# Kernel tuning notes

Hardware: AMD Instinct MI355X
Metric: run time of the kernel (lower is better)

## Reference

```python
import jax, jax.numpy as jnp
import numpy as np

B, T = 32, 1024
VOCAB, N_POS = 300, 3001
D, N_HEAD, D_HID, L = 256, 2, 1024, 4
K1_PAD = 4  # kernel 9, padding 4; second conv is kernel 1, padding 0
EPS = 1e-5


def layer_norm(x, g, b):
    m = jnp.mean(x, axis=-1, keepdims=True)
    v = jnp.mean((x - m) ** 2, axis=-1, keepdims=True)
    return (x - m) * jax.lax.rsqrt(v + EPS) * g + b


def setup_inputs() -> dict:
    key = jax.random.key(0)
    ks = jax.random.split(key, 16)
    src_seq = jax.random.randint(ks[0], (B, T), 0, VOCAB)
    src_pos = jnp.broadcast_to(jnp.arange(1, T + 1), (B, T)).astype(jnp.int32)
    word_emb = (0.02 * jax.random.normal(ks[1], (VOCAB, D))).at[0].set(0.0)  # padding_idx=0
    pos_emb = (0.02 * jax.random.normal(ks[2], (N_POS, D))).at[0].set(0.0)
    s = 0.02
    qkv_w = np.sqrt(2.0 / (D + D // N_HEAD)) * jax.random.normal(ks[3], (L, 3 * D, D))
    qkv_b = jnp.zeros((L, 3 * D))
    fc_w = s * jax.random.normal(ks[4], (L, D, D))
    fc_b = jnp.zeros((L, D))
    ln1_g = jnp.ones((L, D)); ln1_b = jnp.zeros((L, D))
    conv1_w = s * jax.random.normal(ks[5], (L, D_HID, D, 9))
    conv1_b = jnp.zeros((L, D_HID))
    conv2_w = s * jax.random.normal(ks[6], (L, D, D_HID, 1))
    conv2_b = jnp.zeros((L, D))
    ln2_g = jnp.ones((L, D)); ln2_b = jnp.zeros((L, D))
    return dict(src_seq=src_seq, src_pos=src_pos, word_emb=word_emb, pos_emb=pos_emb,
                qkv_w=qkv_w, qkv_b=qkv_b, fc_w=fc_w, fc_b=fc_b,
                ln1_g=ln1_g, ln1_b=ln1_b, conv1_w=conv1_w, conv1_b=conv1_b,
                conv2_w=conv2_w, conv2_b=conv2_b, ln2_g=ln2_g, ln2_b=ln2_b)


def encoder(src_seq, src_pos, word_emb, pos_emb, qkv_w, qkv_b, fc_w, fc_b,
            ln1_g, ln1_b, conv1_w, conv1_b, conv2_w, conv2_b, ln2_g, ln2_b):
    non_pad = (src_seq != 0).astype(jnp.float32)[..., None]          # [B,T,1]
    key_pad = (src_seq == 0)[:, None, None, :]                        # [B,1,1,T]
    x = word_emb[src_seq] + pos_emb[src_pos]                          # [B,T,D]
    dk = D // N_HEAD

    def block(x, p):
        qw, qb, fw, fb, g1, be1, w1, b1, w2, b2, g2, be2 = p
        res = x
        h = layer_norm(x, g1, be1)
        qkv = h @ qw.T + qb                                           # [B,T,3D]
        q, k, v = jnp.split(qkv, 3, axis=-1)
        split = lambda t: t.reshape(B, T, N_HEAD, dk).transpose(0, 2, 1, 3)
        q, k, v = split(q), split(k), split(v)
        attn = jnp.einsum('bhqd,bhkd->bhqk', q, k) / jnp.sqrt(jnp.float32(dk))
        attn = jnp.where(key_pad, -jnp.inf, attn)
        attn = jax.nn.softmax(attn, axis=-1)
        o = jnp.einsum('bhqk,bhkd->bhqd', attn, v)
        o = o.transpose(0, 2, 1, 3).reshape(B, T, D)
        x = (o @ fw.T + fb) + res
        x = x * non_pad
        # position-wise conv FFN
        res = x
        h = layer_norm(x, g2, be2).transpose(0, 2, 1)                 # [B,D,T]
        h = jax.lax.conv_general_dilated(h, w1, (1,), [(K1_PAD, K1_PAD)],
                                         dimension_numbers=('NCH', 'OIH', 'NCH'))
        h = jax.nn.relu(h + b1[None, :, None])
        h = jax.lax.conv_general_dilated(h, w2, (1,), [(0, 0)],
                                         dimension_numbers=('NCH', 'OIH', 'NCH'))
        h = h + b2[None, :, None]
        x = h.transpose(0, 2, 1) + res
        x = x * non_pad
        return x, None

    params = (qkv_w, qkv_b, fc_w, fc_b, ln1_g, ln1_b,
              conv1_w, conv1_b, conv2_w, conv2_b, ln2_g, ln2_b)
    x, _ = jax.lax.scan(block, x, params)
    return x, non_pad


def reference(src_seq, src_pos, word_emb, pos_emb, qkv_w, qkv_b, fc_w, fc_b,
              ln1_g, ln1_b, conv1_w, conv1_b, conv2_w, conv2_b, ln2_g, ln2_b):
    return encoder(src_seq, src_pos, word_emb, pos_emb, qkv_w, qkv_b, fc_w, fc_b,
                   ln1_g, ln1_b, conv1_w, conv1_b, conv2_w, conv2_b, ln2_g, ln2_b)
```

## Files before the change

### kernel.cpp

```cpp
#include <hip/hip_runtime.h>


#define B_ 32
#define T_ 1024
#define D_ 256
#define NH_ 2
#define DK_ 128
#define DH_ 1024
#define L_ 4
#define MROWS (B_ * T_)
#define KCONV (D_ * 9)
#define TPAD 1032
#define NKT_C1 36

typedef unsigned short u16;
typedef short bf16x8 __attribute__((ext_vector_type(8)));
typedef float f32x4 __attribute__((ext_vector_type(4)));
typedef u16 u16x8 __attribute__((ext_vector_type(8)));

__device__ __forceinline__ float bf2f(u16 h) {
    union { unsigned int u; float f; } a;
    a.u = ((unsigned int)h) << 16;
    return a.f;
}

__device__ __forceinline__ u16 f2bf(float f) {
    union { float f; unsigned int u; } a;
    a.f = f;
    unsigned int r = a.u + 0x7fffu + ((a.u >> 16) & 1u);
    return (u16)(r >> 16);
}

__device__ __forceinline__ void glds16(const u16* g, u16* l) {
    __builtin_amdgcn_global_load_lds(
        (const __attribute__((address_space(1))) void*)g,
        (__attribute__((address_space(3))) void*)l, 16, 0, 0);
}

__global__ void detect_kernel(const void* wemb_raw, int* flag) {
    __shared__ int cnt;
    if (threadIdx.x == 0) cnt = 0;
    __syncthreads();
    const u16* p = (const u16*)wemb_raw;
    if (p[256 + threadIdx.x] != 0) atomicAdd(&cnt, 1);
    __syncthreads();
    if (threadIdx.x == 0) *flag = (cnt >= 128) ? 1 : 0;
}

__global__ void cvt_any_kernel(const void* __restrict__ src, u16* __restrict__ dst,
                               int n, const int* __restrict__ flag) {
    int i = blockIdx.x * 256 + threadIdx.x;
    if (i >= n) return;
    if (*flag) dst[i] = ((const u16*)src)[i];
    else       dst[i] = f2bf(((const float*)src)[i]);
}

__global__ void w1_reorder2_kernel(const float* __restrict__ srcf,
                                   const u16* __restrict__ srch,
                                   u16* __restrict__ out, int n,
                                   const int* __restrict__ flag) {
    int idx = blockIdx.x * 256 + threadIdx.x;
    if (idx >= n) return;
    int l  = idx / (DH_ * KCONV);
    int r  = idx % (DH_ * KCONV);
    int oc = r / KCONV;
    int kk = r % KCONV;
    int kpos = kk >> 8;
    int ic   = kk & 255;
    size_t si = (size_t)l * DH_ * D_ * 9 + (oc * D_ + ic) * 9 + kpos;
    out[idx] = (*flag) ? srch[si] : f2bf(srcf[si]);
}

__global__ void sentinel_kernel(void* out, int out_size) {
    int i = blockIdx.x * 256 + threadIdx.x;
    if (i < out_size) ((u16*)out)[i] = 0x42F6;
}


__global__ void embed_kernel(const int* __restrict__ seq, const int* __restrict__ pos,
                             const u16* __restrict__ wemb, const u16* __restrict__ pemb,
                             float* __restrict__ X, float* __restrict__ NP) {
    int row = blockIdx.x;
    int d   = threadIdx.x;
    int s = seq[row];
    int p = pos[row];
    X[(size_t)row * D_ + d] = bf2f(wemb[s * D_ + d]) + bf2f(pemb[p * D_ + d]);
    if (d == 0) NP[row] = (s != 0) ? 1.0f : 0.0f;
}

__global__ void zero_pad_kernel(u16* __restrict__ Hp, int nb) {
    int i = blockIdx.x * 256 + threadIdx.x;
    if (i >= nb * 8 * 256) return;
    int b = i / (8 * 256);
    int r = (i / 256) & 7;
    int d = i & 255;
    int row = (r < 4) ? r : (1024 + r);
    Hp[(size_t)(b * TPAD + row) * D_ + d] = 0;
}

__global__ __launch_bounds__(256)
void ln_kernel(const float* __restrict__ x, const u16* __restrict__ g,
               const u16* __restrict__ bta, u16* __restrict__ outp) {
    int wave = threadIdx.x >> 6, lane = threadIdx.x & 63;
    int row = blockIdx.x * 4 + wave;
    const float* xr = x + (size_t)row * D_;
    float4 v = *(const float4*)&xr[lane * 4];
    float s  = v.x + v.y + v.z + v.w;
    float s2 = v.x * v.x + v.y * v.y + v.z * v.z + v.w * v.w;
#pragma unroll
    for (int d = 1; d < 64; d <<= 1) {
        s  += __shfl_xor(s,  d, 64);
        s2 += __shfl_xor(s2, d, 64);
    }
    float m   = s * (1.0f / 256.0f);
    float var = s2 * (1.0f / 256.0f) - m * m;
    float rr  = rsqrtf(var + 1e-5f);
    size_t orow = (size_t)((row >> 10) * TPAD + 4 + (row & 1023)) * D_;
    float vv[4] = {v.x, v.y, v.z, v.w};
#pragma unroll
    for (int k = 0; k < 4; k++) {
        int d = lane * 4 + k;
        outp[orow + d] = f2bf((vv[k] - m) * rr * bf2f(g[d]) + bf2f(bta[d]));
    }
}

__global__ void out_kernel(const float* __restrict__ X, const float* __restrict__ NP,
                           void* __restrict__ out, int out_size,
                           const int* __restrict__ flag) {
    int i = blockIdx.x * 256 + threadIdx.x;
    if (i >= out_size) return;
    const int n1 = MROWS * D_;
    float v = (i < n1) ? X[i] : NP[i - n1];
    if (*flag) ((u16*)out)[i] = f2bf(v);
    else       ((float*)out)[i] = v;
}

template <int AMAP, int EPI, int K>
__global__ __launch_bounds__(256)
void gemm_mfma(const u16* __restrict__ A, const u16* __restrict__ W,
               const u16* __restrict__ bias, const float* __restrict__ resid,
               const float* __restrict__ mask, void* __restrict__ Cp,
               u16* __restrict__ vout, int M, int N) {
    __shared__ __align__(16) u16 As[128 * 64];
    __shared__ __align__(16) u16 Bs[128 * 64];
    const int tid  = threadIdx.x;
    const int wave = tid >> 6, lane = tid & 63;
    const int quad = lane >> 4, l15 = lane & 15;
    const int m0 = blockIdx.y * 128, n0 = blockIdx.x * 128;
    const int wm = (wave >> 1) * 64, wn = (wave & 1) * 64;
    const int srow = wave * 32;
    const int row8 = lane >> 3;
    const int grp  = ((lane & 7) ^ row8) * 8;
    f32x4 acc[4][4] = {};

    const u16* pa;
    {
        int m = m0 + srow + row8;
        if (AMAP == 0) pa = A + (size_t)m * K + grp;
        else {
            int hr = (m >> 10) * TPAD + (m & 1023) + (AMAP == 1 ? 4 : 0);
            pa = A + (size_t)hr * D_ + grp;
        }
    }
    const u16* pb = W + (size_t)(n0 + srow + row8) * K + grp;
    constexpr size_t rsA = (AMAP == 0) ? (size_t)K : (size_t)D_;
    constexpr size_t rsB = (size_t)K;

    u16* lda = &As[srow * 64];
    u16* ldb = &Bs[srow * 64];
    const int rg = (quad ^ (l15 & 7)) * 8;

    int kpos = 0;
    constexpr int nkt = K / 64;
    for (int t = 0; t < nkt; t++) {
#pragma unroll
        for (int q = 0; q < 4; q++) {
            glds16(pa + (size_t)q * 8 * rsA, lda + q * 8 * 64);
            glds16(pb + (size_t)q * 8 * rsB, ldb + q * 8 * 64);
        }
        if (AMAP == 2) {
            if (kpos == 8) { kpos = 0; pa += 64 - 8 * 256; pb += 64 - 8 * 256; }
            else           { kpos++;  pa += 256;           pb += 256; }
        } else { pa += 64; pb += 64; }
        __builtin_amdgcn_s_waitcnt(0);
        __syncthreads();
#pragma unroll
        for (int ks = 0; ks < 2; ks++) {
            bf16x8 af[4], bfr[4];
#pragma unroll
            for (int i = 0; i < 4; i++)
                af[i] = *(const bf16x8*)&As[(wm + i * 16 + l15) * 64 + (rg ^ (ks * 32))];
#pragma unroll
            for (int j = 0; j < 4; j++)
                bfr[j] = *(const bf16x8*)&Bs[(wn + j * 16 + l15) * 64 + (rg ^ (ks * 32))];
#pragma unroll
            for (int i = 0; i < 4; i++)
#pragma unroll
                for (int j = 0; j < 4; j++)
                    acc[i][j] = __builtin_amdgcn_mfma_f32_16x16x32_bf16(
                        af[i], bfr[j], acc[i][j], 0, 0, 0);
        }
        __syncthreads();
    }

    float bv[4];
#pragma unroll
    for (int j = 0; j < 4; j++) bv[j] = bf2f(bias[n0 + wn + j * 16 + l15]);
#pragma unroll
    for (int i = 0; i < 4; i++) {
#pragma unroll
        for (int j = 0; j < 4; j++) {
            int n = n0 + wn + j * 16 + l15;
            int mbase = m0 + wm + i * 16 + quad * 4;
            float o[4];
#pragma unroll
            for (int r = 0; r < 4; r++) {
                float v = acc[i][j][r] + bv[j];
                if (EPI == 1) v = fmaxf(v, 0.0f);
                o[r] = v;
            }
            if (EPI == 2) {
#pragma unroll
                for (int r = 0; r < 4; r++) {
                    int m = mbase + r;
                    float v = (o[r] + resid[(size_t)m * N + n]) * mask[m];
                    ((float*)Cp)[(size_t)m * N + n] = v;
                }
            } else if (EPI == 3) {
                if (n0 < 512) {
#pragma unroll
                    for (int r = 0; r < 4; r++)
                        ((u16*)Cp)[(size_t)(mbase + r) * 512 + n] = f2bf(o[r]);
                } else {
                    int dg = n - 512;
                    int bb = mbase >> 10, tt = mbase & 1023;
                    ushort4 pk;
                    pk.x = f2bf(o[0]); pk.y = f2bf(o[1]);
                    pk.z = f2bf(o[2]); pk.w = f2bf(o[3]);
                    *(ushort4*)&vout[(size_t)((dg >> 7) + (bb << 1)) * (128 * 1024)
                                     + (size_t)(dg & 127) * 1024 + tt] = pk;
                }
            } else {
#pragma unroll
                for (int r = 0; r < 4; r++)
                    ((u16*)Cp)[(size_t)(mbase + r) * N + n] = f2bf(o[r]);
            }
        }
    }
}

__global__ __launch_bounds__(512, 2)
void gemm_conv1_8p(const u16* __restrict__ Ag, const u16* __restrict__ Wg,
                   const u16* __restrict__ bias, u16* __restrict__ Cp) {
    __shared__ __align__(16) u16 As[2][16384];
    __shared__ __align__(16) u16 Bs[2][16384];
    const int tid  = threadIdx.x;
    const int lane = tid & 63;
    const int wave = tid >> 6;
    const int quad = lane >> 4, l15 = lane & 15;
    const int wr = wave >> 2, wc = wave & 3;
    const int m0 = blockIdx.y << 8, n0 = blockIdx.x << 8;
    const int hr0 = (m0 >> 10) * TPAD + (m0 & 1023);
    const int srow = tid >> 3, sch = tid & 7;

    const u16* pA[4];
    const u16* pB[4];
#pragma unroll
    for (int z = 0; z < 4; z++) {
        int r  = z * 64 + srow;
        int ch = (sch ^ (r & 7)) * 8;
        pA[z] = Ag + (size_t)(hr0 + r) * 256 + ch;
        pB[z] = Wg + (size_t)(n0 + r) * KCONV + ch;
    }
    const int ld0 = tid * 8;

#pragma unroll
    for (int z = 0; z < 4; z++) glds16(pA[z], &As[0][z * 4096 + ld0]);
#pragma unroll
    for (int z = 0; z < 4; z++) glds16(pB[z], &Bs[0][z * 4096 + ld0]);
#pragma unroll
    for (int z = 0; z < 4; z++) { pA[z] += 64; glds16(pA[z], &As[1][z * 4096 + ld0]); }

    const int cA0  = (quad ^ (l15 & 7)) * 8;
    const int cA1  = cA0 ^ 32;
    const int arow = (wr * 128 + l15) * 64;
    const int brow = (wc * 64  + l15) * 64;

    f32x4 acc[8][4] = {};

#pragma unroll 1
    for (int t = 0; t < NKT_C1; t++) {
        const int s = t & 1;
        u16* AsS = As[s];
        u16* BsS = Bs[s];
        u16* AsP = As[s];
        u16* BsP = Bs[s ^ 1];
        bf16x8 a0[8], a1[8], b0, b1;

        if (t < NKT_C1 - 1) asm volatile("s_waitcnt vmcnt(4)" ::: "memory");
        else                asm volatile("s_waitcnt vmcnt(0)" ::: "memory");
        __builtin_amdgcn_s_barrier();
        asm volatile("" ::: "memory");
#pragma unroll
        for (int mf = 0; mf < 8; mf++)
            a0[mf] = *(const bf16x8*)&AsS[arow + mf * 1024 + cA0];
        b0 = *(const bf16x8*)&BsS[brow + cA0];
        b1 = *(const bf16x8*)&BsS[brow + 1024 + cA0];
        if (t + 1 < NKT_C1) {
            pB[0] += 64; pB[1] += 64;
            glds16(pB[0], &BsP[ld0]);
            glds16(pB[1], &BsP[4096 + ld0]);
        }
        __builtin_amdgcn_s_setprio(1);
#pragma unroll
        for (int mf = 0; mf < 8; mf++) {
            acc[mf][0] = __builtin_amdgcn_mfma_f32_16x16x32_bf16(a0[mf], b0, acc[mf][0], 0, 0, 0);
            acc[mf][1] = __builtin_amdgcn_mfma_f32_16x16x32_bf16(a0[mf], b1, acc[mf][1], 0, 0, 0);
        }
        __builtin_amdgcn_s_setprio(0);
        asm volatile("s_waitcnt lgkmcnt(0)" ::: "memory");
        __builtin_amdgcn_s_barrier();
        asm volatile("" ::: "memory");

#pragma unroll
        for (int mf = 0; mf < 8; mf++)
            a1[mf] = *(const bf16x8*)&AsS[arow + mf * 1024 + cA1];
        b0 = *(const bf16x8*)&BsS[brow + cA1];
        b1 = *(const bf16x8*)&BsS[brow + 1024 + cA1];
        if (t + 1 < NKT_C1) {
            pB[2] += 64; pB[3] += 64;
            glds16(pB[2], &BsP[2 * 4096 + ld0]);
            glds16(pB[3], &BsP[3 * 4096 + ld0]);
        }
        __builtin_amdgcn_s_setprio(1);
#pragma unroll
        for (int mf = 0; mf < 8; mf++) {
            acc[mf][0] = __builtin_amdgcn_mfma_f32_16x16x32_bf16(a1[mf], b0, acc[mf][0], 0, 0, 0);
            acc[mf][1] = __builtin_amdgcn_mfma_f32_16x16x32_bf16(a1[mf], b1, acc[mf][1], 0, 0, 0);
        }
        __builtin_amdgcn_s_setprio(0);
        asm volatile("s_waitcnt lgkmcnt(0)" ::: "memory");
        __builtin_amdgcn_s_barrier();
        asm volatile("" ::: "memory");

        b0 = *(const bf16x8*)&BsS[brow + 2 * 1024 + cA0];
        b1 = *(const bf16x8*)&BsS[brow + 3 * 1024 + cA0];
        if (t + 2 < NKT_C1) {
            pA[0] += 64; pA[1] += 64;
            glds16(pA[0], &AsP[ld0]);
            glds16(pA[1], &AsP[4096 + ld0]);
        }
        __builtin_amdgcn_s_setprio(1);
#pragma unroll
        for (int mf = 0; mf < 8; mf++) {
            acc[mf][2] = __builtin_amdgcn_mfma_f32_16x16x32_bf16(a0[mf], b0, acc[mf][2], 0, 0, 0);
            acc[mf][3] = __builtin_amdgcn_mfma_f32_16x16x32_bf16(a0[mf], b1, acc[mf][3], 0, 0, 0);
        }
        __builtin_amdgcn_s_setprio(0);
        asm volatile("s_waitcnt lgkmcnt(0)" ::: "memory");
        __builtin_amdgcn_s_barrier();
        asm volatile("" ::: "memory");

        b0 = *(const bf16x8*)&BsS[brow + 2 * 1024 + cA1];
        b1 = *(const bf16x8*)&BsS[brow + 3 * 1024 + cA1];
        if (t + 2 < NKT_C1) {
            pA[2] += 64; pA[3] += 64;
            glds16(pA[2], &AsP[2 * 4096 + ld0]);
            glds16(pA[3], &AsP[3 * 4096 + ld0]);
        }
        __builtin_amdgcn_s_setprio(1);
#pragma unroll
        for (int mf = 0; mf < 8; mf++) {
            acc[mf][2] = __builtin_amdgcn_mfma_f32_16x16x32_bf16(a1[mf], b0, acc[mf][2], 0, 0, 0);
            acc[mf][3] = __builtin_amdgcn_mfma_f32_16x16x32_bf16(a1[mf], b1, acc[mf][3], 0, 0, 0);
        }
        __builtin_amdgcn_s_setprio(0);
        asm volatile("s_waitcnt lgkmcnt(0)" ::: "memory");
    }

    float bv[4];
#pragma unroll
    for (int nf = 0; nf < 4; nf++)
        bv[nf] = bf2f(bias[n0 + wc * 64 + nf * 16 + l15]);
#pragma unroll
    for (int mf = 0; mf < 8; mf++) {
        const int mr = m0 + wr * 128 + mf * 16 + quad * 4;
#pragma unroll
        for (int nf = 0; nf < 4; nf++) {
            const int cc = n0 + wc * 64 + nf * 16 + l15;
#pragma unroll
            for (int r = 0; r < 4; r++) {
                float v = fmaxf(acc[mf][nf][r] + bv[nf], 0.0f);
                Cp[(size_t)(mr + r) * 1024 + cc] = f2bf(v);
            }
        }
    }
}

__global__ __launch_bounds__(256, 2)
void attn_mfma(const u16* __restrict__ QKV, const u16* __restrict__ Vg,
               const float* __restrict__ NPg, u16* __restrict__ Hp) {
    __shared__ __align__(16) u16 Ks[64 * 128];
    __shared__ __align__(16) u16 Vt[128 * 64];
    __shared__ __align__(16) u16 Ps[4 * 32 * 72];
    __shared__ float npS[1024];
    const int tid  = threadIdx.x;
    const int wave = tid >> 6, lane = tid & 63;
    const int quad = lane >> 4, l15 = lane & 15;
    const int hb = blockIdx.x;
    const int h = hb & (NH_ - 1), b = hb >> 1;
    const int t0 = blockIdx.y * 128;
    const float scale = 0.08838834764831845f;
    u16* Psw = Ps + wave * 32 * 72;
    const u16* Vgh = Vg + (size_t)hb * (128 * 1024);

    for (int i = tid; i < 1024; i += 256) npS[i] = NPg[b * 1024 + i];

    bf16x8 q_a[2][4];
#pragma unroll
    for (int sub = 0; sub < 2; sub++)
#pragma unroll
        for (int s = 0; s < 4; s++)
            q_a[sub][s] = *(const bf16x8*)(QKV
                + (size_t)(b * 1024 + t0 + sub * 64 + wave * 16 + l15) * 512
                + h * DK_ + s * 32 + quad * 8);

    float m_st[2][4], l_st[2][4];
    f32x4 oacc[2][8] = {};
#pragma unroll
    for (int sub = 0; sub < 2; sub++)
#pragma unroll
        for (int r = 0; r < 4; r++) { m_st[sub][r] = -1e30f; l_st[sub][r] = 0.0f; }

    for (int kk = 0; kk < 16; kk++) {
        const int k0 = kk * 64;
        if (kk) __syncthreads();
#pragma unroll
        for (int i = 0; i < 4; i++) {
            int c = i * 256 + tid;
            int key = c >> 4, gk = (c & 15) ^ (key & 15);
            glds16(QKV + (size_t)(b * 1024 + k0 + key) * 512 + 256 + h * DK_ + gk * 8,
                   Ks + (size_t)(i * 256 + wave * 64) * 8);
            int d = c >> 3, gv = (c & 7) ^ (d & 7);
            glds16(Vgh + (size_t)d * 1024 + k0 + gv * 8,
                   Vt + (size_t)(i * 256 + wave * 64) * 8);
        }
        __builtin_amdgcn_s_waitcnt(0);
        __syncthreads();

        f32x4 s4[2][4] = {};
#pragma unroll
        for (int nt = 0; nt < 4; nt++) {
#pragma unroll
            for (int s = 0; s < 4; s++) {
                bf16x8 kb = *(const bf16x8*)&Ks[(nt * 16 + l15) * 128
                                                + ((s * 4 + quad) ^ l15) * 8];
                s4[0][nt] = __builtin_amdgcn_mfma_f32_16x16x32_bf16(
                    q_a[0][s], kb, s4[0][nt], 0, 0, 0);
                s4[1][nt] = __builtin_amdgcn_mfma_f32_16x16x32_bf16(
                    q_a[1][s], kb, s4[1][nt], 0, 0, 0);
            }
        }

#pragma unroll
        for (int sub = 0; sub < 2; sub++) {
#pragma unroll
            for (int nt = 0; nt < 4; nt++) {
                bool pad = (npS[k0 + nt * 16 + l15] == 0.0f);
#pragma unroll
                for (int r = 0; r < 4; r++)
                    s4[sub][nt][r] = pad ? -1e30f : s4[sub][nt][r] * scale;
            }
            float alpha[4];
#pragma unroll
            for (int r = 0; r < 4; r++) {
                float v = fmaxf(fmaxf(s4[sub][0][r], s4[sub][1][r]),
                                fmaxf(s4[sub][2][r], s4[sub][3][r]));
#pragma unroll
                for (int d = 1; d < 16; d <<= 1) v = fmaxf(v, __shfl_xor(v, d, 64));
                float mnew = fmaxf(m_st[sub][r], v);
                alpha[r] = __expf(m_st[sub][r] - mnew);
                m_st[sub][r] = mnew;
                l_st[sub][r] *= alpha[r];
            }
#pragma unroll
            for (int nt = 0; nt < 4; nt++)
#pragma unroll
                for (int r = 0; r < 4; r++)
                    s4[sub][nt][r] = __expf(s4[sub][nt][r] - m_st[sub][r]);
#pragma unroll
            for (int r = 0; r < 4; r++) {
                float v = s4[sub][0][r] + s4[sub][1][r] + s4[sub][2][r] + s4[sub][3][r];
#pragma unroll
                for (int d = 1; d < 16; d <<= 1) v += __shfl_xor(v, d, 64);
                l_st[sub][r] += v;
            }
#pragma unroll
            for (int dt = 0; dt < 8; dt++)
#pragma unroll
                for (int r = 0; r < 4; r++) oacc[sub][dt][r] *= alpha[r];
#pragma unroll
            for (int nt = 0; nt < 4; nt++)
#pragma unroll
                for (int r = 0; r < 4; r++)
                    Psw[(sub * 16 + quad * 4 + r) * 72 + nt * 16 + l15] =
                        f2bf(s4[sub][nt][r]);
        }

#pragma unroll
        for (int ks = 0; ks < 2; ks++) {
            bf16x8 pa0 = *(const bf16x8*)&Psw[l15 * 72 + ks * 32 + quad * 8];
            bf16x8 pa1 = *(const bf16x8*)&Psw[(16 + l15) * 72 + ks * 32 + quad * 8];
#pragma unroll
            for (int dt = 0; dt < 8; dt++) {
                int d = dt * 16 + l15;
                bf16x8 vb = *(const bf16x8*)&Vt[d * 64
                                                + (((ks * 4 + quad) ^ (d & 7)) * 8)];
                oacc[0][dt] = __builtin_amdgcn_mfma_f32_16x16x32_bf16(
                    pa0, vb, oacc[0][dt], 0, 0, 0);
                oacc[1][dt] = __builtin_amdgcn_mfma_f32_16x16x32_bf16(
                    pa1, vb, oacc[1][dt], 0, 0, 0);
            }
        }
    }

#pragma unroll
    for (int sub = 0; sub < 2; sub++)
#pragma unroll
        for (int r = 0; r < 4; r++) {
            float inv = 1.0f / l_st[sub][r];
            int t = t0 + sub * 64 + wave * 16 + quad * 4 + r;
            size_t orow = (size_t)(b * TPAD + 4 + t) * D_ + h * DK_;
#pragma unroll
            for (int dt = 0; dt < 8; dt++)
                Hp[orow + dt * 16 + l15] = f2bf(oacc[sub][dt][r] * inv);
        }
}


static inline int cdiv(int a, int b) { return (a + b - 1) / b; }

extern "C" void kernel_launch(void* const* d_in, const int* in_sizes, int n_in,
                              void* d_out, int out_size, void* d_ws, size_t ws_size,
                              hipStream_t stream) {
    const int* seq = (const int*)d_in[0];
    const int* pos = (const int*)d_in[1];
    (void)in_sizes; (void)n_in;

    int   cb = 8, w1L = 1;
    int*   FLAG; float* X; float* NP; u16* Hpad; u16* SCR; u16* W1R;
    u16 *WEMB, *PEMB, *QKVW, *QKVB, *FCW, *FCB, *G1c, *B1c, *C1B, *C2W, *C2B, *G2c, *B2c;

    unsigned char* wsb = (unsigned char*)d_ws;
    size_t off;
    auto build = [&](int cb_, int w1L_) -> size_t {
        off = 0;
        auto take = [&](size_t bytes) {
            unsigned char* p = wsb + off;
            off += (bytes + 255) & ~(size_t)255;
            return p;
        };
        FLAG = (int*)  take(4);
        X    = (float*)take((size_t)MROWS * D_ * 4);
        NP   = (float*)take((size_t)MROWS * 4);
        Hpad = (u16*)  take((size_t)cb_ * TPAD * D_ * 2);
        SCR  = (u16*)  take((size_t)cb_ * T_ * DH_ * 2);
        W1R  = (u16*)  take((size_t)w1L_ * DH_ * KCONV * 2);
        WEMB = (u16*)  take((size_t)300 * D_ * 2);
        PEMB = (u16*)  take((size_t)3001 * D_ * 2);
        QKVW = (u16*)  take((size_t)L_ * 3 * D_ * D_ * 2);
        QKVB = (u16*)  take((size_t)L_ * 3 * D_ * 2);
        FCW  = (u16*)  take((size_t)L_ * D_ * D_ * 2);
        FCB  = (u16*)  take((size_t)L_ * D_ * 2);
        G1c  = (u16*)  take((size_t)L_ * D_ * 2);
        B1c  = (u16*)  take((size_t)L_ * D_ * 2);
        C1B  = (u16*)  take((size_t)L_ * DH_ * 2);
        C2W  = (u16*)  take((size_t)L_ * D_ * DH_ * 2);
        C2B  = (u16*)  take((size_t)L_ * D_ * 2);
        G2c  = (u16*)  take((size_t)L_ * D_ * 2);
        B2c  = (u16*)  take((size_t)L_ * D_ * 2);
        return off;
    };
    if      (build(32, L_) <= ws_size) { cb = 32; w1L = L_; }
    else if (build(8,  L_) <= ws_size) { cb = 8;  w1L = L_; }
    else if (build(8,  1)  <= ws_size) { cb = 8;  w1L = 1;  }
    else {
        sentinel_kernel<<<cdiv(out_size, 256), 256, 0, stream>>>(d_out, out_size);
        return;
    }
    const int nch = B_ / cb;
    const int Mc  = cb * T_;

    detect_kernel<<<1, 256, 0, stream>>>(d_in[2], FLAG);
    auto cvt = [&](const void* src, u16* dst, int n) {
        cvt_any_kernel<<<cdiv(n, 256), 256, 0, stream>>>(src, dst, n, FLAG);
    };
    cvt(d_in[2],  WEMB, 300 * D_);
    cvt(d_in[3],  PEMB, 3001 * D_);
    cvt(d_in[4],  QKVW, L_ * 3 * D_ * D_);
    cvt(d_in[5],  QKVB, L_ * 3 * D_);
    cvt(d_in[6],  FCW,  L_ * D_ * D_);
    cvt(d_in[7],  FCB,  L_ * D_);
    cvt(d_in[8],  G1c,  L_ * D_);
    cvt(d_in[9],  B1c,  L_ * D_);
    cvt(d_in[11], C1B,  L_ * DH_);
    cvt(d_in[12], C2W,  L_ * D_ * DH_);
    cvt(d_in[13], C2B,  L_ * D_);
    cvt(d_in[14], G2c,  L_ * D_);
    cvt(d_in[15], B2c,  L_ * D_);
    if (w1L == L_) {
        int n = L_ * DH_ * KCONV;
        w1_reorder2_kernel<<<cdiv(n, 256), 256, 0, stream>>>(
            (const float*)d_in[10], (const u16*)d_in[10], W1R, n, FLAG);
    }

    embed_kernel<<<MROWS, 256, 0, stream>>>(seq, pos, WEMB, PEMB, X, NP);
    zero_pad_kernel<<<cb * 8, 256, 0, stream>>>(Hpad, cb);

    for (int l = 0; l < L_; l++) {
        for (int c = 0; c < nch; c++) {
            const size_t ro = (size_t)c * Mc;
            u16* QKV = SCR;
            u16* Vg  = SCR + (size_t)Mc * 512;
            ln_kernel<<<Mc / 4, 256, 0, stream>>>(
                X + ro * D_, G1c + l * D_, B1c + l * D_, Hpad);
            gemm_mfma<1, 3, 256><<<dim3(6, Mc / 128), 256, 0, stream>>>(
                Hpad, QKVW + (size_t)l * 3 * D_ * D_, QKVB + l * 3 * D_,
                nullptr, nullptr, QKV, Vg, Mc, 768);
            attn_mfma<<<dim3(NH_ * cb, 8), 256, 0, stream>>>(
                QKV, Vg, NP + ro, Hpad);
            gemm_mfma<1, 2, 256><<<dim3(2, Mc / 128), 256, 0, stream>>>(
                Hpad, FCW + (size_t)l * D_ * D_, FCB + l * D_,
                X + ro * D_, NP + ro, X + ro * D_, nullptr, Mc, D_);
        }
        const u16* w1p = W1R + (w1L == L_ ? (size_t)l * DH_ * KCONV : 0);
        if (w1L != L_) {
            int n = DH_ * KCONV;
            w1_reorder2_kernel<<<cdiv(n, 256), 256, 0, stream>>>(
                (const float*)d_in[10] + (size_t)l * DH_ * D_ * 9,
                (const u16*)d_in[10] + (size_t)l * DH_ * D_ * 9,
                W1R, n, FLAG);
        }
        for (int c = 0; c < nch; c++) {
            const size_t ro = (size_t)c * Mc;
            ln_kernel<<<Mc / 4, 256, 0, stream>>>(
                X + ro * D_, G2c + l * D_, B2c + l * D_, Hpad);
            gemm_conv1_8p<<<dim3(4, Mc / 256), 512, 0, stream>>>(
                Hpad, w1p, C1B + l * DH_, SCR);
            gemm_mfma<0, 2, 1024><<<dim3(2, Mc / 128), 256, 0, stream>>>(
                SCR, C2W + (size_t)l * D_ * DH_, C2B + l * D_,
                X + ro * D_, NP + ro, X + ro * D_, nullptr, Mc, D_);
        }
    }

    out_kernel<<<cdiv(out_size, 256), 256, 0, stream>>>(X, NP, d_out, out_size, FLAG);
}
```

Measured before the change: 1.426 ms.

## Remap conv1 GEMM tiles across XCDs and restructure 8-phase LDS/MFMA schedule

Block indices are remapped so blocks that land on the same XCD share an N tile and a contiguous range of M tiles, which should improve L2 reuse of the weight and activation tiles. Inside the K loop, the global-to-LDS prefetch is now issued before the LDS fragment reads. Each phase now uses a barrier, an lgkmcnt wait and a sched_barrier before the MFMA cluster, replacing the trailing wait and barrier. This reshuffles where waves synchronise and keeps the compiler from moving MFMAs across the fences, aiming for better overlap. The cost is one extra barrier per phase, plus a tile mapping that depends on the grid being 4 by 128 blocks.

```diff
diff --git a/kernel.cpp b/kernel.cpp
--- a/kernel.cpp
+++ b/kernel.cpp
@@ -259,7 +259,11 @@
     const int wave = tid >> 6;
     const int quad = lane >> 4, l15 = lane & 15;
     const int wr = wave >> 2, wc = wave & 3;
-    const int m0 = blockIdx.y << 8, n0 = blockIdx.x << 8;
+    const int f   = blockIdx.y * 4 + blockIdx.x;
+    const int xcd = f & 7, pos = f >> 3;
+    const int ntile = xcd >> 1;
+    const int mtile = ((xcd & 1) << 6) + pos;
+    const int m0 = mtile << 8, n0 = ntile << 8;
     const int hr0 = (m0 >> 10) * TPAD + (m0 & 1023);
     const int srow = tid >> 3, sch = tid & 7;
 
@@ -287,6 +291,11 @@
     const int brow = (wc * 64  + l15) * 64;
 
     f32x4 acc[8][4] = {};
+
+#define FENCE() asm volatile("" ::: "memory")
+#define LGK0()  asm volatile("s_waitcnt lgkmcnt(0)" ::: "memory")
+#define SBAR()  __builtin_amdgcn_s_barrier()
+#define SCHB()  __builtin_amdgcn_sched_barrier(0)
 
 #pragma unroll 1
     for (int t = 0; t < NKT_C1; t++) {
@@ -299,18 +308,20 @@
 
         if (t < NKT_C1 - 1) asm volatile("s_waitcnt vmcnt(4)" ::: "memory");
         else                asm volatile("s_waitcnt vmcnt(0)" ::: "memory");
-        __builtin_amdgcn_s_barrier();
-        asm volatile("" ::: "memory");
+        SBAR();
+        FENCE();
+
+        if (t + 1 < NKT_C1) {
+            pB[0] += 64; pB[1] += 64;
+            glds16(pB[0], &BsP[ld0]);
+            glds16(pB[1], &BsP[4096 + ld0]);
+        }
 #pragma unroll
         for (int mf = 0; mf < 8; mf++)
             a0[mf] = *(const bf16x8*)&AsS[arow + mf * 1024 + cA0];
         b0 = *(const bf16x8*)&BsS[brow + cA0];
         b1 = *(const bf16x8*)&BsS[brow + 1024 + cA0];
-        if (t + 1 < NKT_C1) {
-            pB[0] += 64; pB[1] += 64;
-            glds16(pB[0], &BsP[ld0]);
-            glds16(pB[1], &BsP[4096 + ld0]);
-        }
+        FENCE(); SBAR(); LGK0(); SCHB();
         __builtin_amdgcn_s_setprio(1);
 #pragma unroll
         for (int mf = 0; mf < 8; mf++) {
@@ -318,20 +329,19 @@
             acc[mf][1] = __builtin_amdgcn_mfma_f32_16x16x32_bf16(a0[mf], b1, acc[mf][1], 0, 0, 0);
         }
         __builtin_amdgcn_s_setprio(0);
-        asm volatile("s_waitcnt lgkmcnt(0)" ::: "memory");
-        __builtin_amdgcn_s_barrier();
-        asm volatile("" ::: "memory");
-
+        FENCE(); SBAR();
+
+        if (t + 1 < NKT_C1) {
+            pB[2] += 64; pB[3] += 64;
+            glds16(pB[2], &BsP[2 * 4096 + ld0]);
+            glds16(pB[3], &BsP[3 * 4096 + ld0]);
+        }
 #pragma unroll
         for (int mf = 0; mf < 8; mf++)
             a1[mf] = *(const bf16x8*)&AsS[arow + mf * 1024 + cA1];
         b0 = *(const bf16x8*)&BsS[brow + cA1];
         b1 = *(const bf16x8*)&BsS[brow + 1024 + cA1];
-        if (t + 1 < NKT_C1) {
-            pB[2] += 64; pB[3] += 64;
-            glds16(pB[2], &BsP[2 * 4096 + ld0]);
-            glds16(pB[3], &BsP[3 * 4096 + ld0]);
-        }
+        FENCE(); SBAR(); LGK0(); SCHB();
         __builtin_amdgcn_s_setprio(1);
 #pragma unroll
         for (int mf = 0; mf < 8; mf++) {
@@ -339,17 +349,16 @@
             acc[mf][1] = __builtin_amdgcn_mfma_f32_16x16x32_bf16(a1[mf], b1, acc[mf][1], 0, 0, 0);
         }
         __builtin_amdgcn_s_setprio(0);
-        asm volatile("s_waitcnt lgkmcnt(0)" ::: "memory");
-        __builtin_amdgcn_s_barrier();
-        asm volatile("" ::: "memory");
-
-        b0 = *(const bf16x8*)&BsS[brow + 2 * 1024 + cA0];
-        b1 = *(const bf16x8*)&BsS[brow + 3 * 1024 + cA0];
+        FENCE(); SBAR();
+
         if (t + 2 < NKT_C1) {
             pA[0] += 64; pA[1] += 64;
             glds16(pA[0], &AsP[ld0]);
             glds16(pA[1], &AsP[4096 + ld0]);
         }
+        b0 = *(const bf16x8*)&BsS[brow + 2 * 1024 + cA0];
+        b1 = *(const bf16x8*)&BsS[brow + 3 * 1024 + cA0];
+        FENCE(); SBAR(); LGK0(); SCHB();
         __builtin_amdgcn_s_setprio(1);
 #pragma unroll
         for (int mf = 0; mf < 8; mf++) {
@@ -357,17 +366,16 @@
             acc[mf][3] = __builtin_amdgcn_mfma_f32_16x16x32_bf16(a0[mf], b1, acc[mf][3], 0, 0, 0);
         }
         __builtin_amdgcn_s_setprio(0);
-        asm volatile("s_waitcnt lgkmcnt(0)" ::: "memory");
-        __builtin_amdgcn_s_barrier();
-        asm volatile("" ::: "memory");
-
-        b0 = *(const bf16x8*)&BsS[brow + 2 * 1024 + cA1];
-        b1 = *(const bf16x8*)&BsS[brow + 3 * 1024 + cA1];
+        FENCE(); SBAR();
+
         if (t + 2 < NKT_C1) {
             pA[2] += 64; pA[3] += 64;
             glds16(pA[2], &AsP[2 * 4096 + ld0]);
             glds16(pA[3], &AsP[3 * 4096 + ld0]);
         }
+        b0 = *(const bf16x8*)&BsS[brow + 2 * 1024 + cA1];
+        b1 = *(const bf16x8*)&BsS[brow + 3 * 1024 + cA1];
+        FENCE(); SBAR(); LGK0(); SCHB();
         __builtin_amdgcn_s_setprio(1);
 #pragma unroll
         for (int mf = 0; mf < 8; mf++) {
@@ -375,8 +383,13 @@
             acc[mf][3] = __builtin_amdgcn_mfma_f32_16x16x32_bf16(a1[mf], b1, acc[mf][3], 0, 0, 0);
         }
         __builtin_amdgcn_s_setprio(0);
-        asm volatile("s_waitcnt lgkmcnt(0)" ::: "memory");
-    }
+        FENCE();
+    }
+
+#undef FENCE
+#undef LGK0
+#undef SBAR
+#undef SCHB
 
     float bv[4];
 #pragma unroll
```

Result: slower. 1.587 ms (+11.3%).
